# Performance work log

Hardware: AMD Instinct MI355X
Metric: run time of the kernel (lower is better)

## Reference

```python
import jax, jax.numpy as jnp
import numpy as np

B, C_IN, T = 128, 17, 4096
N = T // 4          # nodes per sample after two MaxPool1d(2)
D_GAT_IN, D_GAT_OUT = 64, 16
NEG_SLOPE = 0.2     # PyG GATConv default leaky_relu slope


def setup_inputs() -> dict:
    key = jax.random.key(0)
    ks = jax.random.split(key, 12)
    s = lambda fan: 1.0 / np.sqrt(fan)
    return {
        "x": jax.random.normal(ks[0], (B, C_IN, T), dtype=jnp.float32),
        "conv1_w": jax.random.normal(ks[1], (32, C_IN, 5), dtype=jnp.float32) * s(C_IN * 5),
        "conv1_b": jax.random.normal(ks[2], (32,), dtype=jnp.float32) * s(C_IN * 5),
        "conv2_w": jax.random.normal(ks[3], (64, 32, 5), dtype=jnp.float32) * s(32 * 5),
        "conv2_b": jax.random.normal(ks[4], (64,), dtype=jnp.float32) * s(32 * 5),
        "gat_w": jax.random.normal(ks[5], (D_GAT_OUT, D_GAT_IN), dtype=jnp.float32) * s(D_GAT_IN),
        "att_src": jax.random.normal(ks[6], (D_GAT_OUT,), dtype=jnp.float32) * s(D_GAT_OUT),
        "att_dst": jax.random.normal(ks[7], (D_GAT_OUT,), dtype=jnp.float32) * s(D_GAT_OUT),
        "gat_b": jax.random.normal(ks[8], (D_GAT_OUT,), dtype=jnp.float32) * s(D_GAT_OUT),
        "fc_w": jax.random.normal(ks[9], (2, D_GAT_OUT), dtype=jnp.float32) * s(D_GAT_OUT),
        "fc_b": jax.random.normal(ks[10], (2,), dtype=jnp.float32) * s(D_GAT_OUT),
    }


def _conv1d(x, w, b):
    y = jax.lax.conv_general_dilated(
        x, w, window_strides=(1,), padding=[(2, 2)],
        dimension_numbers=("NCH", "OIH", "NCH"))
    return y + b[None, :, None]


def _maxpool2(x):
    b, c, t = x.shape
    return x.reshape(b, c, t // 2, 2).max(axis=-1)


def reference(x, conv1_w, conv1_b, conv2_w, conv2_b,
              gat_w, att_src, att_dst, gat_b, fc_w, fc_b):
    # CNN front-end (dropout is identity in eval)
    h = _maxpool2(jax.nn.relu(_conv1d(x, conv1_w, conv1_b)))
    h = _maxpool2(jax.nn.relu(_conv1d(h, conv2_w, conv2_b)))
    h = h.transpose(0, 2, 1)                       # [B, N, 64]

    # GATConv on a fully-connected graph, batched over samples.
    # PyG GATConv with add_self_loops=True appends self loops even though the
    # dense edge list already contains (i,i), so the self edge appears TWICE
    # in the softmax; we reproduce that exactly.
    hw = jnp.einsum("bnd,od->bno", h, gat_w)       # [B, N, 16]
    s_src = hw @ att_src                            # alpha_j  [B, N]
    s_dst = hw @ att_dst                            # alpha_i  [B, N]
    e = s_dst[:, :, None] + s_src[:, None, :]       # [B, i, j]
    e = jnp.where(e >= 0, e, NEG_SLOPE * e)         # leaky_relu
    w = jnp.exp(e - jax.lax.stop_gradient(e.max(axis=-1, keepdims=True)))
    diag = jnp.diagonal(w, axis1=1, axis2=2)        # duplicated self-loop weight [B, N]
    denom = w.sum(axis=-1) + diag                   # [B, N]
    num = jnp.einsum("bij,bjd->bid", w, hw) + diag[..., None] * hw
    out = num / denom[..., None] + gat_b            # [B, N, 16]

    pooled = out.mean(axis=1)                       # mean over nodes -> [B, 16]
    return pooled @ fc_w.T + fc_b                   # [B, 2]
```

## Files before the change

### kernel.cpp

```cpp
#include <hip/hip_runtime.h>
#include <cstddef>

#define BATCH 128
#define T1 4096
#define P1 2048
#define T2 2048
#define P2 1024
#define NNODE 1024
#define H1ROWS 2052

#define OFF_H1U  ((size_t)0)
#define OFF_SKI  ((size_t)0)
#define OFF_H2   ((size_t)33619968)
#define OFF_HW   ((size_t)67174400)
#define OFF_SSRC ((size_t)75563008)
#define OFF_SDST ((size_t)76087296)
#define OFF_POOL ((size_t)76611584)
#define OFF_W1P  ((size_t)76619776)
#define OFF_W2P  ((size_t)76640256)
#define OFF_GWT  ((size_t)76701696)

typedef __attribute__((ext_vector_type(8))) short bf16x8;
typedef __attribute__((ext_vector_type(4))) float f32x4;

__device__ __forceinline__ ushort f2bf(float v) {
    uint u = __float_as_uint(v);
    uint r = u + 0x7FFFu + ((u >> 16) & 1u);
    return (ushort)(r >> 16);
}
__device__ __forceinline__ float bf2f(ushort h) {
    return __uint_as_float(((uint)h) << 16);
}

__global__ void prep_kernel(const float* __restrict__ w1, const float* __restrict__ w2,
                            const float* __restrict__ gw,
                            ushort* __restrict__ w1p2, ushort* __restrict__ w2p2,
                            float* __restrict__ gwt, uint* __restrict__ h1u32)
{
    const int idx0 = blockIdx.x * 256 + threadIdx.x;
    const int stride = 32 * 256;
    for (int idx = idx0; idx < 10240; idx += stride) {
        int kk = idx >> 11, q = idx & 2047;
        int ks = q >> 10, q2 = q & 1023;
        int o = q2 >> 9, r5 = q2 & 511;
        int l15 = r5 >> 5, ke = r5 & 31;
        int oc = o * 16 + l15, kp = ks * 32 + ke;
        ushort r = 0;
        if (kp < 51) {
            int c = (kp < 17) ? kp : (kp < 34 ? kp - 17 : kp - 34);
            float v = w1[(oc * 17 + c) * 5 + kk];
            ushort hi = f2bf(v);
            r = (kp < 34) ? hi : f2bf(v - bf2f(hi));
        }
        w1p2[idx] = r;
    }
    for (int idx = idx0; idx < 30720; idx += stride) {
        int kk = idx / 6144, rem = idx % 6144;
        int ks = rem >> 11, q2 = rem & 2047;
        int o = q2 >> 9, r5 = q2 & 511;
        int l15 = r5 >> 5, c = r5 & 31;
        int oc = o * 16 + l15;
        float v = w2[(oc * 32 + c) * 5 + kk];
        ushort hi = f2bf(v);
        w2p2[idx] = (ks < 2) ? hi : f2bf(v - bf2f(hi));
    }
    for (int idx = idx0; idx < 1024; idx += stride) {
        int d = idx >> 4, o = idx & 15;
        gwt[idx] = gw[o * 64 + d];
    }
    for (int idx = idx0; idx < 16384; idx += stride) {
        int b = idx >> 7, rr = (idx >> 5) & 3, col = idx & 31;
        int row = (rr < 2) ? rr : (2048 + rr);
        h1u32[((size_t)b * H1ROWS + row) * 32 + col] = 0;
    }
}

__global__ __launch_bounds__(256, 4) void conv1_mfma(
    const float* __restrict__ x, const ushort* __restrict__ w1p2,
    const float* __restrict__ bias, ushort* __restrict__ h1u)
{
    __shared__ ushort sx[260 * 72];
    const int tid = threadIdx.x;
    const int b = blockIdx.y;
    const int tb = blockIdx.x * 256;

    const float* xb = x + (size_t)b * (17 * T1);
    for (int idx = tid; idx < 260 * 17; idx += 256) {
        int r = idx % 260, c = idx / 260;
        int t = tb + r - 2;
        float v = (t >= 0 && t < T1) ? xb[c * T1 + t] : 0.0f;
        ushort hi = f2bf(v);
        ushort lo = f2bf(v - bf2f(hi));
        sx[r * 72 + c] = hi; sx[r * 72 + 17 + c] = lo; sx[r * 72 + 34 + c] = hi;
    }
    for (int idx = tid; idx < 260 * 13; idx += 256) {
        int r = idx / 13, c = 51 + idx % 13;
        sx[r * 72 + c] = 0;
    }
    __syncthreads();

    const int lane = tid & 63;
    const int wv = __builtin_amdgcn_readfirstlane(tid >> 6);
    const int l15 = lane & 15;
    const int kq = lane >> 4;
    f32x4 acc[4][2];
#pragma unroll
    for (int p = 0; p < 4; p++)
#pragma unroll
        for (int o = 0; o < 2; o++) acc[p][o] = (f32x4){0.f, 0.f, 0.f, 0.f};

    const ushort* wb = w1p2 + l15 * 32 + kq * 8;
#pragma unroll
    for (int kk = 0; kk < 5; kk++) {
#pragma unroll
        for (int ks = 0; ks < 2; ks++) {
            bf16x8 B0 = *(const bf16x8*)(wb + (kk * 2 + ks) * 1024);
            bf16x8 B1 = *(const bf16x8*)(wb + (kk * 2 + ks) * 1024 + 512);
#pragma unroll
            for (int p = 0; p < 4; p++) {
                int row = wv * 64 + p * 16 + l15 + kk;
                bf16x8 a = *(const bf16x8*)&sx[row * 72 + ks * 32 + kq * 8];
                acc[p][0] = __builtin_amdgcn_mfma_f32_16x16x32_bf16(a, B0, acc[p][0], 0, 0, 0);
                acc[p][1] = __builtin_amdgcn_mfma_f32_16x16x32_bf16(a, B1, acc[p][1], 0, 0, 0);
            }
        }
    }
    const float bo0 = bias[l15], bo1 = bias[16 + l15];
    ushort* hb = h1u + (size_t)b * H1ROWS * 64;
    const int pbase = tb / 2 + wv * 32 + kq * 2;
#pragma unroll
    for (int p = 0; p < 4; p++) {
        int pr = pbase + p * 8;
#pragma unroll
        for (int o = 0; o < 2; o++) {
            int oc = o * 16 + l15;
            float bo = o ? bo1 : bo0;
            float v0 = fmaxf(fmaxf(acc[p][o][0], acc[p][o][1]) + bo, 0.f);
            float v1 = fmaxf(fmaxf(acc[p][o][2], acc[p][o][3]) + bo, 0.f);
            ushort h0 = f2bf(v0), h1v = f2bf(v1);
            ushort l0 = f2bf(v0 - bf2f(h0)), l1 = f2bf(v1 - bf2f(h1v));
            size_t r0 = (size_t)(pr + 2) * 64, r1 = (size_t)(pr + 3) * 64;
            hb[r0 + oc] = h0; hb[r0 + 32 + oc] = l0;
            hb[r1 + oc] = h1v; hb[r1 + 32 + oc] = l1;
        }
    }
}

__global__ __launch_bounds__(256, 3) void conv2_mfma(
    const ushort* __restrict__ h1u, const ushort* __restrict__ w2p2,
    const float* __restrict__ bias, float* __restrict__ h2)
{
    const int tid = threadIdx.x;
    const int b = blockIdx.y;
    const int tb = blockIdx.x * 256;
    const int lane = tid & 63;
    const int wv = __builtin_amdgcn_readfirstlane(tid >> 6);
    const int l15 = lane & 15;
    const int kq = lane >> 4;

    const ushort* hb = h1u + (size_t)b * H1ROWS * 64;
    const ushort* wb = w2p2 + l15 * 32 + kq * 8;

    f32x4 acc[4][4];
#pragma unroll
    for (int p = 0; p < 4; p++)
#pragma unroll
        for (int o = 0; o < 4; o++) acc[p][o] = (f32x4){0.f, 0.f, 0.f, 0.f};

#pragma unroll
    for (int kk = 0; kk < 5; kk++) {
        bf16x8 aHi[4], aLo[4];
#pragma unroll
        for (int p = 0; p < 4; p++) {
            size_t row = (size_t)(tb + wv * 64 + p * 16 + l15 + kk) * 64;
            aHi[p] = *(const bf16x8*)(hb + row + kq * 8);
            aLo[p] = *(const bf16x8*)(hb + row + 32 + kq * 8);
        }
#pragma unroll
        for (int ks = 0; ks < 3; ks++) {
            bf16x8 B0 = *(const bf16x8*)(wb + (kk * 3 + ks) * 2048);
            bf16x8 B1 = *(const bf16x8*)(wb + (kk * 3 + ks) * 2048 + 512);
            bf16x8 B2 = *(const bf16x8*)(wb + (kk * 3 + ks) * 2048 + 1024);
            bf16x8 B3 = *(const bf16x8*)(wb + (kk * 3 + ks) * 2048 + 1536);
#pragma unroll
            for (int p = 0; p < 4; p++) {
                bf16x8 a = (ks == 1) ? aLo[p] : aHi[p];
                acc[p][0] = __builtin_amdgcn_mfma_f32_16x16x32_bf16(a, B0, acc[p][0], 0, 0, 0);
                acc[p][1] = __builtin_amdgcn_mfma_f32_16x16x32_bf16(a, B1, acc[p][1], 0, 0, 0);
                acc[p][2] = __builtin_amdgcn_mfma_f32_16x16x32_bf16(a, B2, acc[p][2], 0, 0, 0);
                acc[p][3] = __builtin_amdgcn_mfma_f32_16x16x32_bf16(a, B3, acc[p][3], 0, 0, 0);
            }
        }
    }
    float* hb2 = h2 + (size_t)b * P2 * 64;
    const int pbase = tb / 2 + wv * 32 + kq * 2;
#pragma unroll
    for (int p = 0; p < 4; p++) {
        int pr = pbase + p * 8;
#pragma unroll
        for (int o = 0; o < 4; o++) {
            int oc = o * 16 + l15;
            float bo = bias[oc];
            float v0 = fmaxf(fmaxf(acc[p][o][0], acc[p][o][1]) + bo, 0.f);
            float v1 = fmaxf(fmaxf(acc[p][o][2], acc[p][o][3]) + bo, 0.f);
            hb2[(size_t)pr * 64 + oc] = v0;
            hb2[(size_t)(pr + 1) * 64 + oc] = v1;
        }
    }
}

__global__ __launch_bounds__(256, 4) void gat_hw_kernel(
    const float* __restrict__ h2, const float* __restrict__ gwt,
    const float* __restrict__ att_src, const float* __restrict__ att_dst,
    float* __restrict__ hw, float* __restrict__ s_src, float* __restrict__ s_dst)
{
    const int tid = threadIdx.x, b = blockIdx.y;
    const int n = blockIdx.x * 256 + tid;
    const float* row = h2 + ((size_t)b * NNODE + n) * 64;

    float acc[16];
#pragma unroll
    for (int o = 0; o < 16; o++) acc[o] = 0.f;
#pragma unroll
    for (int q = 0; q < 16; q++) {
        float4 h4 = *(const float4*)(row + q * 4);
        float hv[4] = {h4.x, h4.y, h4.z, h4.w};
#pragma unroll
        for (int e = 0; e < 4; e++) {
            const float* wp = &gwt[(q * 4 + e) * 16];
            float4 w0 = *(const float4*)(wp);
            float4 w1 = *(const float4*)(wp + 4);
            float4 w2 = *(const float4*)(wp + 8);
            float4 w3 = *(const float4*)(wp + 12);
            float hvv = hv[e];
            acc[0]  += hvv * w0.x; acc[1]  += hvv * w0.y; acc[2]  += hvv * w0.z; acc[3]  += hvv * w0.w;
            acc[4]  += hvv * w1.x; acc[5]  += hvv * w1.y; acc[6]  += hvv * w1.z; acc[7]  += hvv * w1.w;
            acc[8]  += hvv * w2.x; acc[9]  += hvv * w2.y; acc[10] += hvv * w2.z; acc[11] += hvv * w2.w;
            acc[12] += hvv * w3.x; acc[13] += hvv * w3.y; acc[14] += hvv * w3.z; acc[15] += hvv * w3.w;
        }
    }
    float ss = 0.f, sd = 0.f;
#pragma unroll
    for (int c = 0; c < 16; c++) { ss += acc[c] * att_src[c]; sd += acc[c] * att_dst[c]; }
    float4* hp = (float4*)(hw + ((size_t)b * NNODE + n) * 16);
    hp[0] = make_float4(acc[0], acc[1], acc[2], acc[3]);
    hp[1] = make_float4(acc[4], acc[5], acc[6], acc[7]);
    hp[2] = make_float4(acc[8], acc[9], acc[10], acc[11]);
    hp[3] = make_float4(acc[12], acc[13], acc[14], acc[15]);
    s_src[b * NNODE + n] = ss;
    s_dst[b * NNODE + n] = sd;
}

__global__ __launch_bounds__(256) void rank_kernel(
    const float* __restrict__ s_src, float2* __restrict__ ski)
{
    const int tid = threadIdx.x, b = blockIdx.y;
    const int j = blockIdx.x * 256 + tid;
    const float k = s_src[b * NNODE + j];
    const float4* cand = (const float4*)(s_src + b * NNODE);
    int r = 0;
#pragma unroll 4
    for (int u4 = 0; u4 < 256; u4++) {
        const float4 c = cand[u4];
        const int u = u4 * 4;
        r += (c.x < k || (c.x == k && (u + 0) < j));
        r += (c.y < k || (c.y == k && (u + 1) < j));
        r += (c.z < k || (c.z == k && (u + 2) < j));
        r += (c.w < k || (c.w == k && (u + 3) < j));
    }
    ski[b * NNODE + r] = make_float2(k, __int_as_float(j));
}

__device__ __forceinline__ void accum17(float* L, float wgt, const float4* hj)
{
    float4 a0 = hj[0], a1 = hj[1], a2 = hj[2], a3 = hj[3];
    L[0]  += wgt * a0.x; L[1]  += wgt * a0.y; L[2]  += wgt * a0.z; L[3]  += wgt * a0.w;
    L[4]  += wgt * a1.x; L[5]  += wgt * a1.y; L[6]  += wgt * a1.z; L[7]  += wgt * a1.w;
    L[8]  += wgt * a2.x; L[9]  += wgt * a2.y; L[10] += wgt * a2.z; L[11] += wgt * a2.w;
    L[12] += wgt * a3.x; L[13] += wgt * a3.y; L[14] += wgt * a3.z; L[15] += wgt * a3.w;
    L[16] += wgt;
}

__global__ __launch_bounds__(512) void attn_kernel(
    const float2* __restrict__ ski, const float* __restrict__ s_src,
    const float* __restrict__ s_dst, const float* __restrict__ hw,
    float* __restrict__ pooled)
{
    __shared__ float sPf[1025][17];
    __shared__ float sPg[1025][17];
    __shared__ float sks[1024];
    __shared__ float wsum[8][34];
    __shared__ float sred[8][16];
    const int tid = threadIdx.x, b = blockIdx.x;
    const int lane = tid & 63, wv = tid >> 6;

    const float2 kj0 = ski[b * NNODE + 2 * tid];
    const float2 kj1 = ski[b * NNODE + 2 * tid + 1];
    sks[2 * tid] = kj0.x;
    sks[2 * tid + 1] = kj1.x;
    __syncthreads();
    const float M = sks[1023];
    const float* hwb = hw + (size_t)b * NNODE * 16;
    const int j0 = __float_as_int(kj0.y), j1 = __float_as_int(kj1.y);
    const float f0 = __expf(kj0.x - M), g0 = __expf(0.2f * (kj0.x - M));
    const float f1 = __expf(kj1.x - M), g1 = __expf(0.2f * (kj1.x - M));
    const float4* hj0 = (const float4*)(hwb + (size_t)j0 * 16);
    const float4* hj1 = (const float4*)(hwb + (size_t)j1 * 16);

    float Lf[17], Lg[17];
#pragma unroll
    for (int c = 0; c < 17; c++) { Lf[c] = 0.f; Lg[c] = 0.f; }
    accum17(Lf, f0, hj0); accum17(Lg, g0, hj0);
    accum17(Lf, f1, hj1); accum17(Lg, g1, hj1);

#pragma unroll
    for (int s = 1; s < 64; s <<= 1) {
#pragma unroll
        for (int c = 0; c < 17; c++) {
            float of = __shfl_up(Lf[c], s);
            float og = __shfl_up(Lg[c], s);
            if (lane >= s) { Lf[c] += of; Lg[c] += og; }
        }
    }
    if (lane == 63) {
#pragma unroll
        for (int c = 0; c < 17; c++) { wsum[wv][c] = Lf[c]; wsum[wv][17 + c] = Lg[c]; }
    }
#pragma unroll
    for (int c = 0; c < 17; c++) {
        float ef = __shfl_up(Lf[c], 1);
        float eg = __shfl_up(Lg[c], 1);
        Lf[c] = (lane == 0) ? 0.f : ef;
        Lg[c] = (lane == 0) ? 0.f : eg;
    }
    __syncthreads();
#pragma unroll
    for (int c = 0; c < 17; c++) {
        float bf = 0.f, bg = 0.f;
        for (int w2 = 0; w2 < wv; w2++) { bf += wsum[w2][c]; bg += wsum[w2][17 + c]; }
        Lf[c] += bf; Lg[c] += bg;
    }

    const int p0 = 2 * tid;
#pragma unroll
    for (int c = 0; c < 17; c++) { sPf[p0][c] = Lf[c]; sPg[p0][c] = Lg[c]; }
    accum17(Lf, f0, hj0); accum17(Lg, g0, hj0);
#pragma unroll
    for (int c = 0; c < 17; c++) { sPf[p0 + 1][c] = Lf[c]; sPg[p0 + 1][c] = Lg[c]; }
    accum17(Lf, f1, hj1); accum17(Lg, g1, hj1);
    if (tid == 511) {
#pragma unroll
        for (int c = 0; c < 17; c++) { sPf[1024][c] = Lf[c]; sPg[1024][c] = Lg[c]; }
    }
    __syncthreads();

    float r[16];
#pragma unroll
    for (int c = 0; c < 16; c++) r[c] = 0.f;
#pragma unroll
    for (int e = 0; e < 2; e++) {
        const int i = e * 512 + tid;
        const float sdi = s_dst[b * NNODE + i];
        const float ssi = s_src[b * NNODE + i];
        const float eM = sdi + M;
        const float m_i = (eM >= 0.f) ? eM : 0.2f * eM;
        const float th = -sdi;
        int lo = 0, hi2 = 1024;
        while (lo < hi2) { int mid = (lo + hi2) >> 1; if (sks[mid] < th) lo = mid + 1; else hi2 = mid; }

        const float A  = __expf(eM - m_i);
        const float Bc = __expf(0.2f * eM - m_i);
        float acc[17];
#pragma unroll
        for (int c = 0; c < 17; c++) acc[c] = A * (sPf[1024][c] - sPf[lo][c]) + Bc * sPg[lo][c];

        float e2 = sdi + ssi;
        float el = (e2 >= 0.f) ? e2 : 0.2f * e2;
        float wii = __expf(el - m_i);
        const float4* hi4 = (const float4*)(hwb + (size_t)i * 16);
        accum17(acc, wii, hi4);

        float inv = 1.0f / acc[16];
#pragma unroll
        for (int c = 0; c < 16; c++) r[c] += acc[c] * inv;
    }
#pragma unroll
    for (int s = 32; s > 0; s >>= 1) {
#pragma unroll
        for (int c = 0; c < 16; c++) r[c] += __shfl_down(r[c], s);
    }
    if (lane == 0) {
#pragma unroll
        for (int c = 0; c < 16; c++) sred[wv][c] = r[c];
    }
    __syncthreads();
    if (tid < 16) {
        float t = 0.f;
#pragma unroll
        for (int w2 = 0; w2 < 8; w2++) t += sred[w2][tid];
        pooled[b * 16 + tid] = t;
    }
}

__global__ void final_kernel(
    const float* __restrict__ pooled, const float* __restrict__ gat_b,
    const float* __restrict__ fc_w, const float* __restrict__ fc_b,
    float* __restrict__ out)
{
    int b = threadIdx.x;
    if (b >= BATCH) return;
    float o0 = fc_b[0], o1 = fc_b[1];
#pragma unroll
    for (int d = 0; d < 16; d++) {
        float pv = pooled[b * 16 + d] * (1.0f / 1024.0f) + gat_b[d];
        o0 += pv * fc_w[d];
        o1 += pv * fc_w[16 + d];
    }
    out[2 * b] = o0;
    out[2 * b + 1] = o1;
}

extern "C" void kernel_launch(void* const* d_in, const int* in_sizes, int n_in,
                              void* d_out, int out_size, void* d_ws, size_t ws_size,
                              hipStream_t stream)
{
    (void)in_sizes; (void)n_in; (void)out_size; (void)ws_size;
    const float* x       = (const float*)d_in[0];
    const float* conv1_w = (const float*)d_in[1];
    const float* conv1_b = (const float*)d_in[2];
    const float* conv2_w = (const float*)d_in[3];
    const float* conv2_b = (const float*)d_in[4];
    const float* gat_w   = (const float*)d_in[5];
    const float* att_src = (const float*)d_in[6];
    const float* att_dst = (const float*)d_in[7];
    const float* gat_b   = (const float*)d_in[8];
    const float* fc_w    = (const float*)d_in[9];
    const float* fc_b    = (const float*)d_in[10];
    float* out = (float*)d_out;

    char* ws = (char*)d_ws;
    ushort* h1u   = (ushort*)(ws + OFF_H1U);
    float*  h2    = (float*)(ws + OFF_H2);
    float*  hw    = (float*)(ws + OFF_HW);
    ushort* w1p2  = (ushort*)(ws + OFF_W1P);
    ushort* w2p2  = (ushort*)(ws + OFF_W2P);
    float*  gwt   = (float*)(ws + OFF_GWT);
    float*  ssrc  = (float*)(ws + OFF_SSRC);
    float*  sdst  = (float*)(ws + OFF_SDST);
    float*  pool  = (float*)(ws + OFF_POOL);
    float2* ski   = (float2*)(ws + OFF_SKI);

    hipLaunchKernelGGL(prep_kernel, dim3(32), dim3(256), 0, stream,
                       conv1_w, conv2_w, gat_w, w1p2, w2p2, gwt, (uint*)h1u);
    hipLaunchKernelGGL(conv1_mfma, dim3(16, BATCH), dim3(256), 0, stream,
                       x, w1p2, conv1_b, h1u);
    hipLaunchKernelGGL(conv2_mfma, dim3(8, BATCH), dim3(256), 0, stream,
                       h1u, w2p2, conv2_b, h2);
    hipLaunchKernelGGL(gat_hw_kernel, dim3(4, BATCH), dim3(256), 0, stream,
                       h2, gwt, att_src, att_dst, hw, ssrc, sdst);
    hipLaunchKernelGGL(rank_kernel, dim3(4, BATCH), dim3(256), 0, stream,
                       ssrc, ski);
    hipLaunchKernelGGL(attn_kernel, dim3(BATCH), dim3(512), 0, stream,
                       ski, ssrc, sdst, hw, pool);
    hipLaunchKernelGGL(final_kernel, dim3(1), dim3(128), 0, stream,
                       pool, gat_b, fc_w, fc_b, out);
}
```

Baseline: 238.7 us.

## Move GAT projection to MFMA with split-bf16 h2 and swizzled LDS conv tiles

The GAT linear projection and the attention scores move from a scalar FP32 FMA loop to bf16 MFMA. h2 is stored as hi/lo bf16 pairs, and att_src and att_dst are folded into the weights so that s_src and s_dst come out of the same MFMA pass. conv2 now stages its input rows in XOR-swizzled LDS instead of issuing strided global loads, and conv1 builds each LDS row in registers and writes it with wide swizzled stores. Together these aim to cut ALU work, LDS bank conflicts and global traffic, at the cost of some precision in the folded attention weights (split-bf16 approximates FP32).

```diff
diff --git a/kernel.cpp b/kernel.cpp
--- a/kernel.cpp
+++ b/kernel.cpp
@@ -11,14 +11,15 @@
 
 #define OFF_H1U  ((size_t)0)
 #define OFF_SKI  ((size_t)0)
-#define OFF_H2   ((size_t)33619968)
+#define OFF_H2U  ((size_t)33619968)
 #define OFF_HW   ((size_t)67174400)
 #define OFF_SSRC ((size_t)75563008)
 #define OFF_SDST ((size_t)76087296)
 #define OFF_POOL ((size_t)76611584)
 #define OFF_W1P  ((size_t)76619776)
 #define OFF_W2P  ((size_t)76640256)
-#define OFF_GWT  ((size_t)76701696)
+#define OFF_GB1  ((size_t)76701696)
+#define OFF_GB2  ((size_t)76705792)
 
 typedef __attribute__((ext_vector_type(8))) short bf16x8;
 typedef __attribute__((ext_vector_type(4))) float f32x4;
@@ -34,8 +35,10 @@
 
 __global__ void prep_kernel(const float* __restrict__ w1, const float* __restrict__ w2,
                             const float* __restrict__ gw,
+                            const float* __restrict__ att_src, const float* __restrict__ att_dst,
                             ushort* __restrict__ w1p2, ushort* __restrict__ w2p2,
-                            float* __restrict__ gwt, uint* __restrict__ h1u32)
+                            ushort* __restrict__ gb1, ushort* __restrict__ gb2,
+                            uint* __restrict__ h1u32)
 {
     const int idx0 = blockIdx.x * 256 + threadIdx.x;
     const int stride = 32 * 256;
@@ -64,9 +67,25 @@
         ushort hi = f2bf(v);
         w2p2[idx] = (ks < 2) ? hi : f2bf(v - bf2f(hi));
     }
-    for (int idx = idx0; idx < 1024; idx += stride) {
-        int d = idx >> 4, o = idx & 15;
-        gwt[idx] = gw[o * 64 + d];
+    for (int idx = idx0; idx < 2048; idx += stride) {
+        int j = idx >> 9, l15 = (idx >> 5) & 15, ke = idx & 31;
+        int c = (j & 1) * 32 + ke;
+        float w = gw[l15 * 64 + c];
+        ushort hi = f2bf(w);
+        gb1[idx] = (j < 2) ? hi : f2bf(w - bf2f(hi));
+    }
+    for (int idx = idx0; idx < 2048; idx += stride) {
+        int j = idx >> 9, l15 = (idx >> 5) & 15, ke = idx & 31;
+        ushort r = 0;
+        if (l15 < 2) {
+            int c = (j & 1) * 32 + ke;
+            const float* av = (l15 == 0) ? att_src : att_dst;
+            float a64 = 0.f;
+            for (int o = 0; o < 16; o++) a64 += gw[o * 64 + c] * av[o];
+            ushort hi = f2bf(a64);
+            r = (j < 2) ? hi : f2bf(a64 - bf2f(hi));
+        }
+        gb2[idx] = r;
     }
     for (int idx = idx0; idx < 16384; idx += stride) {
         int b = idx >> 7, rr = (idx >> 5) & 3, col = idx & 31;
@@ -79,23 +98,29 @@
     const float* __restrict__ x, const ushort* __restrict__ w1p2,
     const float* __restrict__ bias, ushort* __restrict__ h1u)
 {
-    __shared__ ushort sx[260 * 72];
+    __shared__ ushort sx[260 * 64];
     const int tid = threadIdx.x;
     const int b = blockIdx.y;
     const int tb = blockIdx.x * 256;
 
     const float* xb = x + (size_t)b * (17 * T1);
-    for (int idx = tid; idx < 260 * 17; idx += 256) {
-        int r = idx % 260, c = idx / 260;
+    for (int r = tid; r < 260; r += 256) {
         int t = tb + r - 2;
-        float v = (t >= 0 && t < T1) ? xb[c * T1 + t] : 0.0f;
-        ushort hi = f2bf(v);
-        ushort lo = f2bf(v - bf2f(hi));
-        sx[r * 72 + c] = hi; sx[r * 72 + 17 + c] = lo; sx[r * 72 + 34 + c] = hi;
-    }
-    for (int idx = tid; idx < 260 * 13; idx += 256) {
-        int r = idx / 13, c = 51 + idx % 13;
-        sx[r * 72 + c] = 0;
+        bool ok = (t >= 0 && t < T1);
+        union { ushort u[64]; uint4 q[8]; } rb;
+#pragma unroll
+        for (int c = 0; c < 17; c++) {
+            float v = ok ? xb[c * T1 + t] : 0.0f;
+            ushort hi = f2bf(v);
+            ushort lo = f2bf(v - bf2f(hi));
+            rb.u[c] = hi; rb.u[17 + c] = lo; rb.u[34 + c] = hi;
+        }
+#pragma unroll
+        for (int i = 51; i < 64; i++) rb.u[i] = 0;
+        uint4* dst = (uint4*)sx;
+#pragma unroll
+        for (int c16 = 0; c16 < 8; c16++)
+            dst[r * 8 + (c16 ^ (r & 7))] = rb.q[c16];
     }
     __syncthreads();
 
@@ -118,8 +143,9 @@
             bf16x8 B1 = *(const bf16x8*)(wb + (kk * 2 + ks) * 1024 + 512);
 #pragma unroll
             for (int p = 0; p < 4; p++) {
-                int row = wv * 64 + p * 16 + l15 + kk;
-                bf16x8 a = *(const bf16x8*)&sx[row * 72 + ks * 32 + kq * 8];
+                int lr = wv * 64 + p * 16 + l15 + kk;
+                int soff = (ks * 32 + kq * 8) ^ ((lr & 7) << 3);
+                bf16x8 a = *(const bf16x8*)&sx[lr * 64 + soff];
                 acc[p][0] = __builtin_amdgcn_mfma_f32_16x16x32_bf16(a, B0, acc[p][0], 0, 0, 0);
                 acc[p][1] = __builtin_amdgcn_mfma_f32_16x16x32_bf16(a, B1, acc[p][1], 0, 0, 0);
             }
@@ -146,21 +172,29 @@
     }
 }
 
-__global__ __launch_bounds__(256, 3) void conv2_mfma(
+__global__ __launch_bounds__(256, 4) void conv2_mfma(
     const ushort* __restrict__ h1u, const ushort* __restrict__ w2p2,
-    const float* __restrict__ bias, float* __restrict__ h2)
-{
+    const float* __restrict__ bias, ushort* __restrict__ h2u)
+{
+    __shared__ ushort sA[260 * 64];
     const int tid = threadIdx.x;
     const int b = blockIdx.y;
     const int tb = blockIdx.x * 256;
+
+    const uint4* src = (const uint4*)(h1u + ((size_t)b * H1ROWS + tb) * 64);
+    uint4* dst = (uint4*)sA;
+    for (int idx = tid; idx < 2080; idx += 256) {
+        int row = idx >> 3, c16 = idx & 7;
+        dst[row * 8 + (c16 ^ (row & 7))] = src[idx];
+    }
+    __syncthreads();
+
     const int lane = tid & 63;
     const int wv = __builtin_amdgcn_readfirstlane(tid >> 6);
     const int l15 = lane & 15;
     const int kq = lane >> 4;
 
-    const ushort* hb = h1u + (size_t)b * H1ROWS * 64;
     const ushort* wb = w2p2 + l15 * 32 + kq * 8;
-
     f32x4 acc[4][4];
 #pragma unroll
     for (int p = 0; p < 4; p++)
@@ -172,9 +206,10 @@
         bf16x8 aHi[4], aLo[4];
 #pragma unroll
         for (int p = 0; p < 4; p++) {
-            size_t row = (size_t)(tb + wv * 64 + p * 16 + l15 + kk) * 64;
-            aHi[p] = *(const bf16x8*)(hb + row + kq * 8);
-            aLo[p] = *(const bf16x8*)(hb + row + 32 + kq * 8);
+            int lr = wv * 64 + p * 16 + l15 + kk;
+            int key = (lr & 7) << 3;
+            aHi[p] = *(const bf16x8*)&sA[lr * 64 + ((kq * 8) ^ key)];
+            aLo[p] = *(const bf16x8*)&sA[lr * 64 + ((32 + kq * 8) ^ key)];
         }
 #pragma unroll
         for (int ks = 0; ks < 3; ks++) {
@@ -192,63 +227,81 @@
             }
         }
     }
-    float* hb2 = h2 + (size_t)b * P2 * 64;
+    ushort* h2b = h2u + (size_t)b * P2 * 128;
     const int pbase = tb / 2 + wv * 32 + kq * 2;
 #pragma unroll
     for (int p = 0; p < 4; p++) {
         int pr = pbase + p * 8;
+        ushort* r0 = h2b + (size_t)pr * 128;
+        ushort* r1 = r0 + 128;
 #pragma unroll
         for (int o = 0; o < 4; o++) {
             int oc = o * 16 + l15;
             float bo = bias[oc];
             float v0 = fmaxf(fmaxf(acc[p][o][0], acc[p][o][1]) + bo, 0.f);
             float v1 = fmaxf(fmaxf(acc[p][o][2], acc[p][o][3]) + bo, 0.f);
-            hb2[(size_t)pr * 64 + oc] = v0;
-            hb2[(size_t)(pr + 1) * 64 + oc] = v1;
-        }
-    }
-}
-
-__global__ __launch_bounds__(256, 4) void gat_hw_kernel(
-    const float* __restrict__ h2, const float* __restrict__ gwt,
-    const float* __restrict__ att_src, const float* __restrict__ att_dst,
-    float* __restrict__ hw, float* __restrict__ s_src, float* __restrict__ s_dst)
+            ushort a0 = f2bf(v0), a1 = f2bf(v1);
+            ushort l0 = f2bf(v0 - bf2f(a0)), l1 = f2bf(v1 - bf2f(a1));
+            r0[oc] = a0; r0[64 + oc] = l0;
+            r1[oc] = a1; r1[64 + oc] = l1;
+        }
+    }
+}
+
+__global__ __launch_bounds__(256) void gat_mfma(
+    const ushort* __restrict__ h2u, const ushort* __restrict__ gb1,
+    const ushort* __restrict__ gb2, float* __restrict__ hw,
+    float* __restrict__ s_src, float* __restrict__ s_dst)
 {
     const int tid = threadIdx.x, b = blockIdx.y;
-    const int n = blockIdx.x * 256 + tid;
-    const float* row = h2 + ((size_t)b * NNODE + n) * 64;
-
-    float acc[16];
-#pragma unroll
-    for (int o = 0; o < 16; o++) acc[o] = 0.f;
-#pragma unroll
-    for (int q = 0; q < 16; q++) {
-        float4 h4 = *(const float4*)(row + q * 4);
-        float hv[4] = {h4.x, h4.y, h4.z, h4.w};
-#pragma unroll
-        for (int e = 0; e < 4; e++) {
-            const float* wp = &gwt[(q * 4 + e) * 16];
-            float4 w0 = *(const float4*)(wp);
-            float4 w1 = *(const float4*)(wp + 4);
-            float4 w2 = *(const float4*)(wp + 8);
-            float4 w3 = *(const float4*)(wp + 12);
-            float hvv = hv[e];
-            acc[0]  += hvv * w0.x; acc[1]  += hvv * w0.y; acc[2]  += hvv * w0.z; acc[3]  += hvv * w0.w;
-            acc[4]  += hvv * w1.x; acc[5]  += hvv * w1.y; acc[6]  += hvv * w1.z; acc[7]  += hvv * w1.w;
-            acc[8]  += hvv * w2.x; acc[9]  += hvv * w2.y; acc[10] += hvv * w2.z; acc[11] += hvv * w2.w;
-            acc[12] += hvv * w3.x; acc[13] += hvv * w3.y; acc[14] += hvv * w3.z; acc[15] += hvv * w3.w;
-        }
-    }
-    float ss = 0.f, sd = 0.f;
-#pragma unroll
-    for (int c = 0; c < 16; c++) { ss += acc[c] * att_src[c]; sd += acc[c] * att_dst[c]; }
-    float4* hp = (float4*)(hw + ((size_t)b * NNODE + n) * 16);
-    hp[0] = make_float4(acc[0], acc[1], acc[2], acc[3]);
-    hp[1] = make_float4(acc[4], acc[5], acc[6], acc[7]);
-    hp[2] = make_float4(acc[8], acc[9], acc[10], acc[11]);
-    hp[3] = make_float4(acc[12], acc[13], acc[14], acc[15]);
-    s_src[b * NNODE + n] = ss;
-    s_dst[b * NNODE + n] = sd;
+    const int lane = tid & 63, wv = tid >> 6, l15 = lane & 15, kq = lane >> 4;
+    const int wbase = blockIdx.x * 256 + wv * 64;
+    const ushort* hb = h2u + ((size_t)b * NNODE + wbase) * 128;
+
+    bf16x8 A[4][4];
+#pragma unroll
+    for (int rg = 0; rg < 4; rg++)
+#pragma unroll
+        for (int ac = 0; ac < 4; ac++)
+            A[rg][ac] = *(const bf16x8*)&hb[(size_t)(rg * 16 + l15) * 128 + ac * 32 + kq * 8];
+
+    bf16x8 B1v[4], B2v[4];
+#pragma unroll
+    for (int j = 0; j < 4; j++) {
+        B1v[j] = *(const bf16x8*)&gb1[j * 512 + l15 * 32 + kq * 8];
+        B2v[j] = *(const bf16x8*)&gb2[j * 512 + l15 * 32 + kq * 8];
+    }
+
+    float* hwb = hw + (size_t)b * NNODE * 16;
+#pragma unroll
+    for (int rg = 0; rg < 4; rg++) {
+        f32x4 h = (f32x4){0.f, 0.f, 0.f, 0.f};
+        f32x4 s = (f32x4){0.f, 0.f, 0.f, 0.f};
+        h = __builtin_amdgcn_mfma_f32_16x16x32_bf16(A[rg][0], B1v[0], h, 0, 0, 0);
+        s = __builtin_amdgcn_mfma_f32_16x16x32_bf16(A[rg][0], B2v[0], s, 0, 0, 0);
+        h = __builtin_amdgcn_mfma_f32_16x16x32_bf16(A[rg][1], B1v[1], h, 0, 0, 0);
+        s = __builtin_amdgcn_mfma_f32_16x16x32_bf16(A[rg][1], B2v[1], s, 0, 0, 0);
+        h = __builtin_amdgcn_mfma_f32_16x16x32_bf16(A[rg][2], B1v[0], h, 0, 0, 0);
+        s = __builtin_amdgcn_mfma_f32_16x16x32_bf16(A[rg][2], B2v[0], s, 0, 0, 0);
+        h = __builtin_amdgcn_mfma_f32_16x16x32_bf16(A[rg][3], B1v[1], h, 0, 0, 0);
+        s = __builtin_amdgcn_mfma_f32_16x16x32_bf16(A[rg][3], B2v[1], s, 0, 0, 0);
+        h = __builtin_amdgcn_mfma_f32_16x16x32_bf16(A[rg][0], B1v[2], h, 0, 0, 0);
+        s = __builtin_amdgcn_mfma_f32_16x16x32_bf16(A[rg][0], B2v[2], s, 0, 0, 0);
+        h = __builtin_amdgcn_mfma_f32_16x16x32_bf16(A[rg][1], B1v[3], h, 0, 0, 0);
+        s = __builtin_amdgcn_mfma_f32_16x16x32_bf16(A[rg][1], B2v[3], s, 0, 0, 0);
+
+        const int n0 = wbase + rg * 16 + kq * 4;
+#pragma unroll
+        for (int reg = 0; reg < 4; reg++)
+            hwb[(size_t)(n0 + reg) * 16 + l15] = h[reg];
+        if (l15 == 0) {
+#pragma unroll
+            for (int reg = 0; reg < 4; reg++) s_src[b * NNODE + n0 + reg] = s[reg];
+        } else if (l15 == 1) {
+#pragma unroll
+            for (int reg = 0; reg < 4; reg++) s_dst[b * NNODE + n0 + reg] = s[reg];
+        }
+    }
 }
 
 __global__ __launch_bounds__(256) void rank_kernel(
@@ -440,24 +493,26 @@
 
     char* ws = (char*)d_ws;
     ushort* h1u   = (ushort*)(ws + OFF_H1U);
-    float*  h2    = (float*)(ws + OFF_H2);
+    ushort* h2u   = (ushort*)(ws + OFF_H2U);
     float*  hw    = (float*)(ws + OFF_HW);
     ushort* w1p2  = (ushort*)(ws + OFF_W1P);
     ushort* w2p2  = (ushort*)(ws + OFF_W2P);
-    float*  gwt   = (float*)(ws + OFF_GWT);
+    ushort* gb1   = (ushort*)(ws + OFF_GB1);
+    ushort* gb2   = (ushort*)(ws + OFF_GB2);
     float*  ssrc  = (float*)(ws + OFF_SSRC);
     float*  sdst  = (float*)(ws + OFF_SDST);
     float*  pool  = (float*)(ws + OFF_POOL);
     float2* ski   = (float2*)(ws + OFF_SKI);
 
     hipLaunchKernelGGL(prep_kernel, dim3(32), dim3(256), 0, stream,
-                       conv1_w, conv2_w, gat_w, w1p2, w2p2, gwt, (uint*)h1u);
+                       conv1_w, conv2_w, gat_w, att_src, att_dst,
+                       w1p2, w2p2, gb1, gb2, (uint*)h1u);
     hipLaunchKernelGGL(conv1_mfma, dim3(16, BATCH), dim3(256), 0, stream,
                        x, w1p2, conv1_b, h1u);
     hipLaunchKernelGGL(conv2_mfma, dim3(8, BATCH), dim3(256), 0, stream,
-                       h1u, w2p2, conv2_b, h2);
-    hipLaunchKernelGGL(gat_hw_kernel, dim3(4, BATCH), dim3(256), 0, stream,
-                       h2, gwt, att_src, att_dst, hw, ssrc, sdst);
+                       h1u, w2p2, conv2_b, h2u);
+    hipLaunchKernelGGL(gat_mfma, dim3(4, BATCH), dim3(256), 0, stream,
+                       h2u, gb1, gb2, hw, ssrc, sdst);
     hipLaunchKernelGGL(rank_kernel, dim3(4, BATCH), dim3(256), 0, stream,
                        ssrc, ski);
     hipLaunchKernelGGL(attn_kernel, dim3(BATCH), dim3(512), 0, stream,
```

After: 213.6 us. 1.12x faster.
